# Kernel optimization log

Measured on AMD Instinct MI355X. Metric: run time of the kernel, lower is better.

Reference implementation:

```python
import jax, jax.numpy as jnp
import numpy as np

B, C, H, W = 16, 2, 768, 768
WIN = 5                      # window_size: maxima kernel AND gauss-fit window
PAD = WIN // 2
HEATMAP_AXIS = 1
THRESHOLD = 0.5
MAX_DET = 393216             # fixed-size pad for data-dependent nonzero()


def setup_inputs() -> dict:
    key = jax.random.key(0)
    # strictly positive heat so log(z) in Guo's fit is well-defined
    x = jax.random.uniform(key, (B, C, H, W), dtype=jnp.float32, minval=1e-4, maxval=1.0)
    return {"x": x}


def _forward(x):
    heat = x[:, HEATMAP_AXIS]                                   # [B,H,W]
    th = jnp.where(heat > THRESHOLD, heat, 0.0)
    # kornia dilation with ones kernel (center zeroed) == max over neighbors excl. center
    padded = jnp.pad(th, ((0, 0), (PAD, PAD), (PAD, PAD)), constant_values=-np.inf)
    dilated = jnp.full(th.shape, -np.inf, th.dtype)
    for dy in range(WIN):
        for dx in range(WIN):
            if dy == PAD and dx == PAD:
                continue
            dilated = jnp.maximum(dilated, padded[:, dy:dy + H, dx:dx + W])
    local_max = (th > dilated).reshape(-1)                      # strict local maxima above threshold
    (flat_idx,) = jnp.nonzero(local_max, size=MAX_DET, fill_value=0)  # row-major, like torch.nonzero
    valid = jnp.arange(MAX_DET) < local_max.sum()
    bidx = flat_idx // (H * W)
    rc = flat_idx % (H * W)
    r = rc // W
    cc = rc % W
    sub = jnp.linspace((-WIN) // 2 + 1, WIN // 2, WIN)
    xs, ys = jnp.meshgrid(sub, sub, indexing='xy')              # xs varies along columns
    xf = xs.reshape(-1).astype(jnp.float32)                     # [K]
    yf = ys.reshape(-1).astype(jnp.float32)
    off = jnp.arange(WIN) - PAD
    off_r = jnp.repeat(off, WIN)                                # row-major window flattening
    off_c = jnp.tile(off, WIN)
    rows = jnp.clip(r[:, None] + off_r[None, :], 0, H - 1)      # clamp at borders
    cols = jnp.clip(cc[:, None] + off_c[None, :], 0, W - 1)
    z = heat[bidx[:, None], rows, cols]                         # [N,K] window intensities
    z = jnp.clip(z, 1e-6, None)                                 # numerical guard for log
    xb = jnp.broadcast_to(xf, z.shape)
    yb = jnp.broadcast_to(yf, z.shape)
    # quadratic basis [1, x, x^2, y, xy, y^2]
    basis = jnp.stack([jnp.ones_like(xb), xb, xb * xb, yb, xb * yb, yb * yb], -1)  # [N,K,6]
    wgt = z * z                                                  # Guo's weights
    Aw = basis * wgt[:, :, None]
    bvec = jnp.log(z) * wgt
    ATA = jnp.einsum('nki,nkj->nij', Aw, Aw)                     # [N,6,6]
    ATb = jnp.einsum('nki,nk->ni', Aw, bvec)                     # [N,6]
    coef = jnp.einsum('nij,nj->ni', jnp.linalg.inv(ATA), ATb)    # [N,6]
    Aq, Bl, Cc = coef[:, [2, 5]], coef[:, [1, 3]], coef[:, [0, 4]]
    good = valid & jnp.all(Aq < 0, axis=-1)                      # concave fit -> real sigma
    g = good[:, None]
    Aq_s = jnp.where(g, Aq, -0.5)                                # guard against NaN at padded slots
    sigma = jnp.sqrt(-1.0 / (2.0 * Aq_s))
    mu = Bl * sigma ** 2
    height = jnp.exp(jnp.where(g, Cc + 0.5 * mu ** 2 / sigma ** 2, 0.0))
    pos = jnp.stack([r, cc], -1).astype(jnp.float32) + mu[:, ::-1]  # maxima_indices + mu[:,[1,0]]
    sigma = jnp.where(g, sigma, 0.0)
    pos = jnp.where(g, pos, 0.0)
    height = jnp.where(g, height, 0.0)
    return sigma, pos, height, good


def reference(x):
    return _forward(x)
```

## Files before the change

kernel.cpp:

```cpp
#include <hip/hip_runtime.h>
#include <hip/hip_bf16.h>
#include <cstdint>

#define BATCH 16
#define HDIM 768
#define WDIM 768
#define HW (HDIM * WDIM)
#define NPIX (BATCH * HW)
#define MAX_DET 393216
#define NWORDS (NPIX / 64)
#define SCAT_BLOCKS 576
#define WPB 256

#define MASK_OFF 0u
#define CNT_OFF  1179648u
#define TOT_OFF  1187840u
#define IDX_OFF  1188096u

#define SIGMA_BASE 0
#define POS_BASE   786432
#define HGT_BASE   1572864
#define GOOD_BASE  2359296

#define TILE_C 256
#define TILE_R 32
#define LDS_C 264
#define LDS_R 36
#define VEC_PER_ROW 66
#define TOT_VEC (LDS_R * VEC_PER_ROW)

__device__ __forceinline__ float fast_logf(float zf) {
    int ib = __float_as_int(zf);
    int e = ((ib >> 23) & 255) - 127;
    float m1 = __int_as_float((ib & 0x007fffff) | 0x3f800000);
    float lg = __builtin_amdgcn_logf(m1);
    return ((float)e + lg) * 0.69314718055994531f;
}

__device__ __forceinline__ double fast_rcp(double d) {
    double r = (double)__builtin_amdgcn_rcpf((float)d);
    r = r * (2.0 - d * r);
    r = r * (2.0 - d * r);
    return r;
}

__global__ __launch_bounds__(256) void mask_kernel(const float* __restrict__ x,
                                                   unsigned long long* __restrict__ mask) {
    __shared__ float lds[LDS_R * LDS_C];
    const int bid = blockIdx.x;
    const int b   = bid / 72;
    const int rem = bid - b * 72;
    const int rt  = rem / 3;
    const int cs  = rem - rt * 3;
    const int r0  = rt * TILE_R;
    const int tid = threadIdx.x;
    const float* heat = x + (size_t)b * (2 * HW) + HW;

    const int colbase = cs * TILE_C - 4;
    #pragma unroll
    for (int i = 0; i < 10; ++i) {
        int idx = i * 256 + tid;
        if (idx < TOT_VEC) {
            int lr = (unsigned)idx / VEC_PER_ROW;
            int q  = idx - lr * VEC_PER_ROW;
            int row = r0 - 2 + lr;
            int col = colbase + 4 * q;
            float4 v = make_float4(0.f, 0.f, 0.f, 0.f);
            if (row >= 0 && row < HDIM && col >= 0 && col <= WDIM - 4) {
                v = *reinterpret_cast<const float4*>(heat + (size_t)row * WDIM + col);
            }
            float4 t;
            t.x = v.x > 0.5f ? v.x : 0.f;
            t.y = v.y > 0.5f ? v.y : 0.f;
            t.z = v.z > 0.5f ? v.z : 0.f;
            t.w = v.w > 0.5f ? v.w : 0.f;
            *reinterpret_cast<float4*>(&lds[lr * LDS_C + 4 * q]) = t;
        }
    }
    __syncthreads();

    const int wv   = tid >> 6;
    const int lane = tid & 63;
    const int lrow0 = wv * 8;

    auto readrow = [&](int ldsrow, float* h5, float* hx, float* tc) {
        const float* p = &lds[ldsrow * LDS_C + 4 * lane];
        float4 a = *reinterpret_cast<const float4*>(p);
        float4 bb = *reinterpret_cast<const float4*>(p + 4);
        float4 cc = *reinterpret_cast<const float4*>(p + 8);
        float t2=a.z,t3=a.w,t4=bb.x,t5=bb.y,t6=bb.z,t7=bb.w,t8=cc.x,t9=cc.y;
        float pp0=fmaxf(t2,t3), pp1=fmaxf(t3,t4), pp2=fmaxf(t4,t5), pp3=fmaxf(t5,t6),
              pp4=fmaxf(t6,t7), pp5=fmaxf(t7,t8), pp6=fmaxf(t8,t9);
        h5[0]=fmaxf(fmaxf(pp0,pp2),t6);  hx[0]=fmaxf(pp0,pp3);  tc[0]=t4;
        h5[1]=fmaxf(fmaxf(pp1,pp3),t7);  hx[1]=fmaxf(pp1,pp4);  tc[1]=t5;
        h5[2]=fmaxf(fmaxf(pp2,pp4),t8);  hx[2]=fmaxf(pp2,pp5);  tc[2]=t6;
        h5[3]=fmaxf(fmaxf(pp3,pp5),t9);  hx[3]=fmaxf(pp3,pp6);  tc[3]=t7;
    };

    float h5r[5][4], hxr[5][4], tcr[5][4];
    #pragma unroll
    for (int j = 0; j < 4; ++j)
        readrow(lrow0 + j, h5r[j], hxr[j], tcr[j]);

    unsigned nibword = 0;
    #pragma unroll
    for (int k = 0; k < 8; ++k) {
        readrow(lrow0 + k + 4, h5r[(k+4)%5], hxr[(k+4)%5], tcr[(k+4)%5]);
        unsigned nib = 0;
        #pragma unroll
        for (int c = 0; c < 4; ++c) {
            float dil = fmaxf(fmaxf(h5r[k%5][c], h5r[(k+1)%5][c]),
                        fmaxf(hxr[(k+2)%5][c],
                        fmaxf(h5r[(k+3)%5][c], h5r[(k+4)%5][c])));
            if (tcr[(k+2)%5][c] > dil) nib |= (1u << c);
        }
        nibword |= nib << (4 * k);
    }

    __syncthreads();
    unsigned* lu = (unsigned*)lds;
    lu[tid] = nibword;
    __syncthreads();
    if (tid < 128) {
        const int wv2 = tid >> 5;
        const int k2  = (tid >> 2) & 7;
        const int wi  = tid & 3;
        const int s   = 4 * k2;
        const uint4* p = (const uint4*)&lu[wv2 * 64 + wi * 16];
        uint4 q0 = p[0], q1 = p[1], q2 = p[2], q3 = p[3];
        unsigned lo = 0, hi = 0;
        lo |= ((q0.x >> s) & 0xFu) << 0;   lo |= ((q0.y >> s) & 0xFu) << 4;
        lo |= ((q0.z >> s) & 0xFu) << 8;   lo |= ((q0.w >> s) & 0xFu) << 12;
        lo |= ((q1.x >> s) & 0xFu) << 16;  lo |= ((q1.y >> s) & 0xFu) << 20;
        lo |= ((q1.z >> s) & 0xFu) << 24;  lo |= ((q1.w >> s) & 0xFu) << 28;
        hi |= ((q2.x >> s) & 0xFu) << 0;   hi |= ((q2.y >> s) & 0xFu) << 4;
        hi |= ((q2.z >> s) & 0xFu) << 8;   hi |= ((q2.w >> s) & 0xFu) << 12;
        hi |= ((q3.x >> s) & 0xFu) << 16;  hi |= ((q3.y >> s) & 0xFu) << 20;
        hi |= ((q3.z >> s) & 0xFu) << 24;  hi |= ((q3.w >> s) & 0xFu) << 28;
        unsigned long long word = (unsigned long long)lo |
                                  ((unsigned long long)hi << 32);
        mask[b * (HW / 64) + (r0 + wv2 * 8 + k2) * 12 + cs * 4 + wi] = word;
    }
}

__global__ __launch_bounds__(WPB) void count_kernel(const unsigned long long* __restrict__ mask,
                                                    int* __restrict__ counts) {
    __shared__ int s[WPB];
    int t = threadIdx.x;
    int w = blockIdx.x * WPB + t;
    s[t] = __popcll(mask[w]);
    __syncthreads();
    for (int off = WPB / 2; off > 0; off >>= 1) {
        if (t < off) s[t] += s[t + off];
        __syncthreads();
    }
    if (t == 0) counts[blockIdx.x] = s[0];
}

__global__ __launch_bounds__(WPB) void scatter_kernel(const unsigned long long* __restrict__ mask,
                                                      const int* __restrict__ counts,
                                                      int* __restrict__ flat_idx,
                                                      int* __restrict__ total) {
    __shared__ int s[WPB];
    __shared__ int blockoff;
    const int t = threadIdx.x;
    const int bid = blockIdx.x;

    int acc = 0;
    for (int i = t; i < bid; i += WPB) acc += counts[i];
    s[t] = acc;
    __syncthreads();
    for (int off = WPB / 2; off > 0; off >>= 1) {
        if (t < off) s[t] += s[t + off];
        __syncthreads();
    }
    if (t == 0) blockoff = s[0];
    __syncthreads();

    if (bid == 0) {
        int a2 = 0;
        for (int i = t; i < SCAT_BLOCKS; i += WPB) a2 += counts[i];
        s[t] = a2;
        __syncthreads();
        for (int off = WPB / 2; off > 0; off >>= 1) {
            if (t < off) s[t] += s[t + off];
            __syncthreads();
        }
        if (t == 0) *total = s[0];
        __syncthreads();
    }

    int w = bid * WPB + t;
    unsigned long long m = mask[w];
    int cnt = __popcll(m);
    s[t] = cnt;
    __syncthreads();
    for (int off = 1; off < WPB; off <<= 1) {
        int add = (t >= off) ? s[t - off] : 0;
        __syncthreads();
        s[t] += add;
        __syncthreads();
    }
    int base = blockoff + s[t] - cnt;
    int idx0 = w << 6;
    while (m) {
        int j = __builtin_ctzll(m);
        if (base < MAX_DET) flat_idx[base] = idx0 + j;
        ++base;
        m &= m - 1;
    }
}

__global__ __launch_bounds__(256) void fit_kernel(const float* __restrict__ x,
                                                  const int* __restrict__ flat_idx,
                                                  const int* __restrict__ total,
                                                  float* __restrict__ out) {
    int n = blockIdx.x * 256 + threadIdx.x;
    int count = *total;
    float sx = 0.f, sy = 0.f, p0 = 0.f, p1 = 0.f, h0 = 0.f, h1 = 0.f, goodf = 0.f;
    if (n < count) {
        int idx = flat_idx[n];
        int b = idx / HW;
        int rc = idx - b * HW;
        int r = rc / WDIM;
        int c = rc - r * WDIM;
        const float* heat = x + (size_t)b * (2 * HW) + HW;

        float M00=0,M10=0,M01=0,M20=0,M11=0,M02=0,M30=0,M21=0,M12=0,M03=0;
        float M40=0,M31=0,M22=0,M13=0,M04=0;
        float N0=0,N1=0,N2=0,N3=0,N4=0,N5=0;
        #pragma unroll
        for (int dy = -2; dy <= 2; ++dy) {
            int rr = min(max(r + dy, 0), HDIM - 1);
            const float* hp = heat + (size_t)rr * WDIM;
            float S0=0,S1=0,S2=0,S3=0,S4=0,T0=0,T1=0,T2=0;
            #pragma unroll
            for (int dx = -2; dx <= 2; ++dx) {
                int cc = min(max(c + dx, 0), WDIM - 1);
                float zf = fmaxf(hp[cc], 1e-6f);
                float z2 = zf * zf;
                float w2 = z2 * z2;
                float wl = w2 * fast_logf(zf);
                const float X = (float)dx;
                S0 += w2; T0 += wl;
                if (dx != 0) {
                    S1 += w2 * X;
                    S2 += w2 * (X * X);
                    S3 += w2 * (X * X * X);
                    S4 += w2 * (X * X * X * X);
                    T1 += wl * X;
                    T2 += wl * (X * X);
                }
            }
            const float Y = (float)dy;
            M00 += S0; M10 += S1; M20 += S2; M30 += S3; M40 += S4;
            N0 += T0; N1 += T1; N2 += T2;
            if (dy != 0) {
                float Y2 = Y * Y, Y3 = Y2 * Y, Y4 = Y2 * Y2;
                M01 += S0 * Y;  M11 += S1 * Y;  M21 += S2 * Y;  M31 += S3 * Y;
                M02 += S0 * Y2; M12 += S1 * Y2; M22 += S2 * Y2;
                M03 += S0 * Y3; M13 += S1 * Y3;
                M04 += S0 * Y4;
                N3 += T0 * Y; N4 += T1 * Y; N5 += T0 * Y2;
            }
        }

        double A[6][7];
        A[0][0]=M00; A[0][1]=M10; A[0][2]=M20; A[0][3]=M01; A[0][4]=M11; A[0][5]=M02; A[0][6]=N0;
        A[1][0]=M10; A[1][1]=M20; A[1][2]=M30; A[1][3]=M11; A[1][4]=M21; A[1][5]=M12; A[1][6]=N1;
        A[2][0]=M20; A[2][1]=M30; A[2][2]=M40; A[2][3]=M21; A[2][4]=M31; A[2][5]=M22; A[2][6]=N2;
        A[3][0]=M01; A[3][1]=M11; A[3][2]=M21; A[3][3]=M02; A[3][4]=M12; A[3][5]=M03; A[3][6]=N3;
        A[4][0]=M11; A[4][1]=M21; A[4][2]=M31; A[4][3]=M12; A[4][4]=M22; A[4][5]=M13; A[4][6]=N4;
        A[5][0]=M02; A[5][1]=M12; A[5][2]=M22; A[5][3]=M03; A[5][4]=M13; A[5][5]=M04; A[5][6]=N5;

        #pragma unroll
        for (int i = 0; i < 6; ++i) {
            double inv = fast_rcp(A[i][i]);
            #pragma unroll
            for (int j = i + 1; j < 7; ++j) A[i][j] *= inv;
            #pragma unroll
            for (int ii = i + 1; ii < 6; ++ii) {
                double f = A[ii][i];
                #pragma unroll
                for (int j = i + 1; j < 7; ++j) A[ii][j] -= f * A[i][j];
            }
        }
        double cv[6];
        #pragma unroll
        for (int i = 5; i >= 0; --i) {
            double v = A[i][6];
            #pragma unroll
            for (int j = i + 1; j < 6; ++j) v -= A[i][j] * cv[j];
            cv[i] = v;
        }

        double aqx = cv[2], aqy = cv[5];
        if (aqx < 0.0 && aqy < 0.0) {
            double sx2 = -0.5 * fast_rcp(aqx);
            double sy2 = -0.5 * fast_rcp(aqy);
            sx2 = fmin(sx2, 1e300);
            sy2 = fmin(sy2, 1e300);
            double sigx = sqrt(sx2), sigy = sqrt(sy2);
            double mux = cv[1] * sx2, muy = cv[3] * sy2;
            sx = (float)sigx;
            sy = (float)sigy;
            p0 = (float)((double)r + muy);
            p1 = (float)((double)c + mux);
            float a0 = (float)((cv[0] + 0.5 * cv[1] * cv[1] * sx2) * 1.4426950408889634);
            float a1 = (float)((cv[4] + 0.5 * cv[3] * cv[3] * sy2) * 1.4426950408889634);
            a0 = fminf(a0, 126.0f);
            a1 = fminf(a1, 126.0f);
            h0 = exp2f(a0);
            h1 = exp2f(a1);
            goodf = 1.0f;
        }
    }
    out[SIGMA_BASE + 2 * n]     = sx;
    out[SIGMA_BASE + 2 * n + 1] = sy;
    out[POS_BASE + 2 * n]       = p0;
    out[POS_BASE + 2 * n + 1]   = p1;
    out[HGT_BASE + 2 * n]       = h0;
    out[HGT_BASE + 2 * n + 1]   = h1;
    out[GOOD_BASE + n]          = goodf;
}

extern "C" void kernel_launch(void* const* d_in, const int* in_sizes, int n_in,
                              void* d_out, int out_size, void* d_ws, size_t ws_size,
                              hipStream_t stream) {
    const float* x = (const float*)d_in[0];
    float* out = (float*)d_out;
    char* ws = (char*)d_ws;

    unsigned long long* mask = (unsigned long long*)(ws + MASK_OFF);
    int* counts  = (int*)(ws + CNT_OFF);
    int* total   = (int*)(ws + TOT_OFF);
    int* flatidx = (int*)(ws + IDX_OFF);

    mask_kernel<<<BATCH * 24 * 3, 256, 0, stream>>>(x, mask);
    count_kernel<<<SCAT_BLOCKS, WPB, 0, stream>>>(mask, counts);
    scatter_kernel<<<SCAT_BLOCKS, WPB, 0, stream>>>(mask, counts, flatidx, total);
    fit_kernel<<<MAX_DET / 256, 256, 0, stream>>>(x, flatidx, total, out);
}
```

Measured before the change: 45.83 us.

## Fuse per-chunk counting into mask kernel and vectorize fit window loads

The mask kernel now popcounts its output words and atomically adds the result into per-row-tile chunk counters. This removes the separate count kernel but adds a memset. The scatter kernel is resized to 384 chunks of 384 words, so each block sums at most 384 prefix counts instead of looping over them. The fit kernel loads each 5-wide window row with two float4 reads for interior columns instead of 25 scalar loads. This adds atomics and extra register use.

```diff
diff --git a/kernel.cpp b/kernel.cpp
--- a/kernel.cpp
+++ b/kernel.cpp
@@ -9,18 +9,6 @@
 #define NPIX (BATCH * HW)
 #define MAX_DET 393216
 #define NWORDS (NPIX / 64)
-#define SCAT_BLOCKS 576
-#define WPB 256
-
-#define MASK_OFF 0u
-#define CNT_OFF  1179648u
-#define TOT_OFF  1187840u
-#define IDX_OFF  1188096u
-
-#define SIGMA_BASE 0
-#define POS_BASE   786432
-#define HGT_BASE   1572864
-#define GOOD_BASE  2359296
 
 #define TILE_C 256
 #define TILE_R 32
@@ -29,6 +17,18 @@
 #define VEC_PER_ROW 66
 #define TOT_VEC (LDS_R * VEC_PER_ROW)
 
+#define NCHUNKS 384
+
+#define WORD_OFF 0u
+#define CNT_OFF  1179648u
+#define TOT_OFF  1181184u
+#define IDX_OFF  1183744u
+
+#define SIGMA_BASE 0
+#define POS_BASE   786432
+#define HGT_BASE   1572864
+#define GOOD_BASE  2359296
+
 __device__ __forceinline__ float fast_logf(float zf) {
     int ib = __float_as_int(zf);
     int e = ((ib >> 23) & 255) - 127;
@@ -45,7 +45,8 @@
 }
 
 __global__ __launch_bounds__(256) void mask_kernel(const float* __restrict__ x,
-                                                   unsigned long long* __restrict__ mask) {
+                                                   unsigned long long* __restrict__ words,
+                                                   int* __restrict__ counts) {
     __shared__ float lds[LDS_R * LDS_C];
     const int bid = blockIdx.x;
     const int b   = bid / 72;
@@ -119,8 +120,11 @@
 
     __syncthreads();
     unsigned* lu = (unsigned*)lds;
+    int* su = (int*)lds + 512;
     lu[tid] = nibword;
     __syncthreads();
+
+    int pc = 0;
     if (tid < 128) {
         const int wv2 = tid >> 5;
         const int k2  = (tid >> 2) & 7;
@@ -139,70 +143,55 @@
         hi |= ((q3.z >> s) & 0xFu) << 24;  hi |= ((q3.w >> s) & 0xFu) << 28;
         unsigned long long word = (unsigned long long)lo |
                                   ((unsigned long long)hi << 32);
-        mask[b * (HW / 64) + (r0 + wv2 * 8 + k2) * 12 + cs * 4 + wi] = word;
-    }
-}
-
-__global__ __launch_bounds__(WPB) void count_kernel(const unsigned long long* __restrict__ mask,
-                                                    int* __restrict__ counts) {
-    __shared__ int s[WPB];
-    int t = threadIdx.x;
-    int w = blockIdx.x * WPB + t;
-    s[t] = __popcll(mask[w]);
-    __syncthreads();
-    for (int off = WPB / 2; off > 0; off >>= 1) {
-        if (t < off) s[t] += s[t + off];
+        words[b * (HW / 64) + (r0 + wv2 * 8 + k2) * 12 + cs * 4 + wi] = word;
+        pc = __popcll(word);
+    }
+    if (tid < 128) su[tid] = pc;
+    __syncthreads();
+    #pragma unroll
+    for (int off = 64; off > 0; off >>= 1) {
+        if (tid < off) su[tid] += su[tid + off];
         __syncthreads();
     }
-    if (t == 0) counts[blockIdx.x] = s[0];
-}
-
-__global__ __launch_bounds__(WPB) void scatter_kernel(const unsigned long long* __restrict__ mask,
+    if (tid == 0) atomicAdd(&counts[b * 24 + rt], su[0]);
+}
+
+__global__ __launch_bounds__(384) void scatter_kernel(const unsigned long long* __restrict__ words,
                                                       const int* __restrict__ counts,
                                                       int* __restrict__ flat_idx,
                                                       int* __restrict__ total) {
-    __shared__ int s[WPB];
+    __shared__ int s[512];
+    __shared__ int s2[384];
     __shared__ int blockoff;
     const int t = threadIdx.x;
-    const int bid = blockIdx.x;
-
-    int acc = 0;
-    for (int i = t; i < bid; i += WPB) acc += counts[i];
-    s[t] = acc;
-    __syncthreads();
-    for (int off = WPB / 2; off > 0; off >>= 1) {
+    const int chunk = blockIdx.x;
+
+    s[t] = (t < chunk) ? counts[t] : 0;
+    if (t < 128) s[384 + t] = 0;
+    __syncthreads();
+    #pragma unroll
+    for (int off = 256; off > 0; off >>= 1) {
         if (t < off) s[t] += s[t + off];
         __syncthreads();
     }
     if (t == 0) blockoff = s[0];
     __syncthreads();
 
-    if (bid == 0) {
-        int a2 = 0;
-        for (int i = t; i < SCAT_BLOCKS; i += WPB) a2 += counts[i];
-        s[t] = a2;
+    unsigned long long m = words[chunk * 384 + t];
+    int pc = __popcll(m);
+    s2[t] = pc;
+    __syncthreads();
+    for (int off = 1; off < 384; off <<= 1) {
+        int add = (t >= off) ? s2[t - off] : 0;
         __syncthreads();
-        for (int off = WPB / 2; off > 0; off >>= 1) {
-            if (t < off) s[t] += s[t + off];
-            __syncthreads();
-        }
-        if (t == 0) *total = s[0];
+        s2[t] += add;
         __syncthreads();
     }
-
-    int w = bid * WPB + t;
-    unsigned long long m = mask[w];
-    int cnt = __popcll(m);
-    s[t] = cnt;
-    __syncthreads();
-    for (int off = 1; off < WPB; off <<= 1) {
-        int add = (t >= off) ? s[t - off] : 0;
-        __syncthreads();
-        s[t] += add;
-        __syncthreads();
-    }
-    int base = blockoff + s[t] - cnt;
-    int idx0 = w << 6;
+    if (chunk == NCHUNKS - 1 && t == 383)
+        *total = blockoff + s2[383];
+
+    int base = blockoff + s2[t] - pc;
+    int idx0 = (chunk * 384 + t) << 6;
     while (m) {
         int j = __builtin_ctzll(m);
         if (base < MAX_DET) flat_idx[base] = idx0 + j;
@@ -216,7 +205,7 @@
                                                   const int* __restrict__ total,
                                                   float* __restrict__ out) {
     int n = blockIdx.x * 256 + threadIdx.x;
-    int count = *total;
+    int count = min(*total, MAX_DET);
     float sx = 0.f, sy = 0.f, p0 = 0.f, p1 = 0.f, h0 = 0.f, h1 = 0.f, goodf = 0.f;
     if (n < count) {
         int idx = flat_idx[n];
@@ -226,18 +215,47 @@
         int c = rc - r * WDIM;
         const float* heat = x + (size_t)b * (2 * HW) + HW;
 
+        float zv[25];
+        if (c >= 2 && c <= WDIM - 3) {
+            const int a   = (c - 2) & ~3;
+            const int ofs = (c - 2) & 3;
+            #pragma unroll
+            for (int dy = 0; dy < 5; ++dy) {
+                int rr = min(max(r + dy - 2, 0), HDIM - 1);
+                const float* hp = heat + (size_t)rr * WDIM + a;
+                float4 u0 = *reinterpret_cast<const float4*>(hp);
+                float4 u1 = *reinterpret_cast<const float4*>(hp + 4);
+                float b0=u0.x, b1=u0.y, b2=u0.z, b3=u0.w;
+                float b4=u1.x, b5=u1.y, b6=u1.z, b7=u1.w;
+                float v0, v1, v2, v3, v4;
+                if (ofs == 0)      { v0=b0; v1=b1; v2=b2; v3=b3; v4=b4; }
+                else if (ofs == 1) { v0=b1; v1=b2; v2=b3; v3=b4; v4=b5; }
+                else if (ofs == 2) { v0=b2; v1=b3; v2=b4; v3=b5; v4=b6; }
+                else               { v0=b3; v1=b4; v2=b5; v3=b6; v4=b7; }
+                zv[dy*5+0]=v0; zv[dy*5+1]=v1; zv[dy*5+2]=v2; zv[dy*5+3]=v3; zv[dy*5+4]=v4;
+            }
+        } else {
+            #pragma unroll
+            for (int dy = 0; dy < 5; ++dy) {
+                int rr = min(max(r + dy - 2, 0), HDIM - 1);
+                const float* hp = heat + (size_t)rr * WDIM;
+                #pragma unroll
+                for (int dx = 0; dx < 5; ++dx) {
+                    int cc = min(max(c + dx - 2, 0), WDIM - 1);
+                    zv[dy * 5 + dx] = hp[cc];
+                }
+            }
+        }
+
         float M00=0,M10=0,M01=0,M20=0,M11=0,M02=0,M30=0,M21=0,M12=0,M03=0;
         float M40=0,M31=0,M22=0,M13=0,M04=0;
         float N0=0,N1=0,N2=0,N3=0,N4=0,N5=0;
         #pragma unroll
         for (int dy = -2; dy <= 2; ++dy) {
-            int rr = min(max(r + dy, 0), HDIM - 1);
-            const float* hp = heat + (size_t)rr * WDIM;
             float S0=0,S1=0,S2=0,S3=0,S4=0,T0=0,T1=0,T2=0;
             #pragma unroll
             for (int dx = -2; dx <= 2; ++dx) {
-                int cc = min(max(c + dx, 0), WDIM - 1);
-                float zf = fmaxf(hp[cc], 1e-6f);
+                float zf = fmaxf(zv[(dy + 2) * 5 + dx + 2], 1e-6f);
                 float z2 = zf * zf;
                 float w2 = z2 * z2;
                 float wl = w2 * fast_logf(zf);
@@ -331,13 +349,14 @@
     float* out = (float*)d_out;
     char* ws = (char*)d_ws;
 
-    unsigned long long* mask = (unsigned long long*)(ws + MASK_OFF);
+    unsigned long long* words = (unsigned long long*)(ws + WORD_OFF);
     int* counts  = (int*)(ws + CNT_OFF);
     int* total   = (int*)(ws + TOT_OFF);
     int* flatidx = (int*)(ws + IDX_OFF);
 
-    mask_kernel<<<BATCH * 24 * 3, 256, 0, stream>>>(x, mask);
-    count_kernel<<<SCAT_BLOCKS, WPB, 0, stream>>>(mask, counts);
-    scatter_kernel<<<SCAT_BLOCKS, WPB, 0, stream>>>(mask, counts, flatidx, total);
+    hipMemsetAsync(ws + CNT_OFF, 0, NCHUNKS * 4, stream);
+
+    mask_kernel<<<BATCH * 24 * 3, 256, 0, stream>>>(x, words, counts);
+    scatter_kernel<<<NCHUNKS, 384, 0, stream>>>(words, counts, flatidx, total);
     fit_kernel<<<MAX_DET / 256, 256, 0, stream>>>(x, flatidx, total, out);
 }
```

After: 55.12 us. +20.3%, slower.
